# Kernel optimization log

Measured on AMD Instinct MI355X. Metric: run time of the kernel, lower is better.

## Reference

```python
import jax, jax.numpy as jnp
import numpy as np

NR, NQ, NH, NV = 256, 64, 64, 4
B = 8192
NDRAW = 12
# zoneout probabilities from __init__ (applied deterministically, eval-mode expectation)
ZO_IJ, ZO_ID, ZO_GJ, ZO_GD = 0.3, 0.2, 0.3, 0.2


def _lin_init(key, fan_in, fan_out):
    kw, kb = jax.random.split(key)
    s = 1.0 / np.sqrt(fan_in)
    W = jax.random.uniform(kw, (fan_in, fan_out), jnp.float32, -s, s)
    b = jax.random.uniform(kb, (fan_out,), jnp.float32, -s, s)
    return W, b


def setup_inputs() -> dict:
    key = jax.random.key(0)
    ks = jax.random.split(key, 16)
    inp = {"ndraw": NDRAW}
    inp["cnd_repr"] = jax.random.normal(ks[0], (B, NR), jnp.float32)
    inp["qry_jrep"] = jax.random.normal(ks[1], (B, NQ), jnp.float32)
    inp["qry_drep"] = jax.random.normal(ks[2], (B, NQ), jnp.float32)
    inp["qry_v"] = jax.random.normal(ks[3], (B, NV), jnp.float32)
    for n in ["hi_j", "ci_j", "oi_j", "hi_d", "ci_d", "oi_d",
              "hg_j", "cg_j", "og_j", "hg_d", "cg_d", "og_d", "ug_j", "ug_d"]:
        inp[n] = jnp.zeros((B, NH), jnp.float32)
    # LSTM cells: W [in+nh, 4*nh]
    inp["W_ij"], inp["b_ij"] = _lin_init(ks[4], NR + NQ + NH + NH, 4 * NH)
    inp["W_id"], inp["b_id"] = _lin_init(ks[5], NR + NQ + NH + NH, 4 * NH)
    inp["W_gj"], inp["b_gj"] = _lin_init(ks[6], NR + NH + NH, 4 * NH)
    inp["W_gd"], inp["b_gd"] = _lin_init(ks[7], NR + NH + NV + NH, 4 * NH)
    # GaussianFactor heads: nh -> (mean, logv)
    inp["W_poj"], inp["b_poj"] = _lin_init(ks[8], NH, 2 * NH)
    inp["W_pod"], inp["b_pod"] = _lin_init(ks[9], NH, 2 * NH)
    inp["W_prj"], inp["b_prj"] = _lin_init(ks[10], NH, 2 * NH)
    inp["W_prd"], inp["b_prd"] = _lin_init(ks[11], NH, 2 * NH)
    # GeneratorDelta: cat(u, h) -> delta
    inp["W_dj"], inp["b_dj"] = _lin_init(ks[12], 2 * NH, NH)
    inp["W_dd"], inp["b_dd"] = _lin_init(ks[13], 2 * NH, NH)
    return inp


def _lstm(x, h, c, W, b, zo):
    g = jnp.concatenate([x, h], axis=1) @ W + b  # [B, 4*NH]
    i, f, gg, o = jnp.split(g, 4, axis=1)
    i, f, o = jax.nn.sigmoid(i), jax.nn.sigmoid(f), jax.nn.sigmoid(o)
    c_new = f * c + i * jnp.tanh(gg)
    h_new = o * jnp.tanh(c_new)
    # deterministic zoneout (expectation form)
    return zo * h + (1.0 - zo) * h_new, zo * c + (1.0 - zo) * c_new, o


def _gauss_stats(h, W, b):
    s = h @ W + b
    mean, logv = jnp.split(s, 2, axis=1)
    return mean, logv


def _delta(u, h, W, b):
    return jax.nn.leaky_relu(jnp.concatenate([u, h], axis=1) @ W + b)


def _forward(ndraw, cnd_repr, qry_jrep, qry_drep, qry_v,
             hi_j, ci_j, oi_j, hi_d, ci_d, oi_d,
             hg_j, cg_j, og_j, hg_d, cg_d, og_d, ug_j, ug_d,
             W_ij, b_ij, W_id, b_id, W_gj, b_gj, W_gd, b_gd,
             W_poj, b_poj, W_pod, b_pod, W_prj, b_prj, W_prd, b_prd,
             W_dj, b_dj, W_dd, b_dd):
    Bn = cnd_repr.shape[0]
    eps_j = jax.random.normal(jax.random.key(1), (ndraw, Bn, NH), jnp.float32)
    eps_d = jax.random.normal(jax.random.key(2), (ndraw, Bn, NH), jnp.float32)

    def step(carry, eps):
        (hi_j, ci_j, oi_j, hi_d, ci_d, oi_d,
         hg_j, cg_j, og_j, hg_d, cg_d, og_d, ug_j, ug_d) = carry
        ej, ed = eps
        # priors from current generator states (sampled z unused in loop)
        pr_m_j, pr_v_j = _gauss_stats(hg_j, W_prj, b_prj)
        pr_m_d, pr_v_d = _gauss_stats(hg_d, W_prd, b_prd)
        # inference states
        inp_ij = jnp.concatenate([cnd_repr, qry_jrep, hg_j], axis=1)
        inp_id = jnp.concatenate([cnd_repr, qry_drep, hg_d], axis=1)
        hi_j, ci_j, oi_j = _lstm(inp_ij, hi_j, ci_j, W_ij, b_ij, ZO_IJ)
        hi_d, ci_d, oi_d = _lstm(inp_id, hi_d, ci_d, W_id, b_id, ZO_ID)
        # posteriors + reparameterized samples
        po_m_j, po_v_j = _gauss_stats(hi_j, W_poj, b_poj)
        po_m_d, po_v_d = _gauss_stats(hi_d, W_pod, b_pod)
        z_j = po_m_j + jnp.exp(0.5 * po_v_j) * ej
        z_d = po_m_d + jnp.exp(0.5 * po_v_d) * ed
        # generator states
        inp_gj = jnp.concatenate([cnd_repr, z_j], axis=1)
        inp_gd = jnp.concatenate([cnd_repr, z_d, qry_v], axis=1)
        hg_j, cg_j, og_j = _lstm(inp_gj, hg_j, cg_j, W_gj, b_gj, ZO_GJ)
        hg_d, cg_d, og_d = _lstm(inp_gd, hg_d, cg_d, W_gd, b_gd, ZO_GD)
        # additive canvas updates
        ug_j = ug_j + _delta(ug_j, hg_j, W_dj, b_dj)
        ug_d = ug_d + _delta(ug_d, hg_d, W_dd, b_dd)
        carry = (hi_j, ci_j, oi_j, hi_d, ci_d, oi_d,
                 hg_j, cg_j, og_j, hg_d, cg_d, og_d, ug_j, ug_d)
        ys = (pr_m_j, pr_v_j, pr_m_d, pr_v_d, po_m_j, po_v_j, po_m_d, po_v_d)
        return carry, ys

    carry0 = (hi_j, ci_j, oi_j, hi_d, ci_d, oi_d,
              hg_j, cg_j, og_j, hg_d, cg_d, og_d, ug_j, ug_d)
    carry, ys = jax.lax.scan(step, carry0, (eps_j, eps_d))
    ug_j_out, ug_d_out = carry[-2], carry[-1]
    # pack: [2 + 8*ndraw, B, NH] (canvases then per-draw prior/posterior stats)
    out = jnp.concatenate([ug_j_out[None], ug_d_out[None]] + list(ys), axis=0)
    return out


def reference(ndraw, cnd_repr, qry_jrep, qry_drep, qry_v,
              hi_j, ci_j, oi_j, hi_d, ci_d, oi_d,
              hg_j, cg_j, og_j, hg_d, cg_d, og_d, ug_j, ug_d,
              W_ij, b_ij, W_id, b_id, W_gj, b_gj, W_gd, b_gd,
              W_poj, b_poj, W_pod, b_pod, W_prj, b_prj, W_prd, b_prd,
              W_dj, b_dj, W_dd, b_dd):
    return _forward(ndraw, cnd_repr, qry_jrep, qry_drep, qry_v,
                    hi_j, ci_j, oi_j, hi_d, ci_d, oi_d,
                    hg_j, cg_j, og_j, hg_d, cg_d, og_d, ug_j, ug_d,
                    W_ij, b_ij, W_id, b_id, W_gj, b_gj, W_gd, b_gd,
                    W_poj, b_poj, W_pod, b_pod, W_prj, b_prj, W_prd, b_prd,
                    W_dj, b_dj, W_dd, b_dd)
```

## Files before the change

kernel.cpp:

```cpp
#include <hip/hip_runtime.h>
#include <hip/hip_bf16.h>


#define RROWS 16

typedef __attribute__((ext_vector_type(8))) short bf16x8;
typedef __attribute__((ext_vector_type(4))) float f32x4;

#define MFMA(A, Bv, C) __builtin_amdgcn_mfma_f32_16x16x32_bf16(A, Bv, C, 0, 0, 0)

#define FR_WI   0
#define FR_WG   32768
#define FR_WPR  65536
#define FR_WPO  73728
#define FR_WD   81920
#define FR_SIDE 90112

__device__ __forceinline__ unsigned short f2bf(float f) {
  unsigned u = __float_as_uint(f);
  return (unsigned short)((u + 0x7FFFu + ((u >> 16) & 1u)) >> 16);
}
__device__ __forceinline__ unsigned pk2(float a, float b) {
  return (unsigned)f2bf(a) | ((unsigned)f2bf(b) << 16);
}
__device__ __forceinline__ float sigf(float x) {
  return 1.0f / (1.0f + __expf(-x));
}
__device__ __forceinline__ float tanh_f(float x) {
  return 1.0f - 2.0f / (__expf(2.0f * x) + 1.0f);
}

__device__ __forceinline__ float eps_threefry(unsigned seed, unsigned idx) {
  unsigned x0 = 0u, x1 = idx;
  const unsigned ks0 = 0u, ks1 = seed, ks2 = seed ^ 0x1BD11BDAu;
  x0 += ks0; x1 += ks1;
#define TF_R(r) { x0 += x1; x1 = (x1 << (r)) | (x1 >> (32 - (r))); x1 ^= x0; }
  TF_R(13) TF_R(15) TF_R(26) TF_R(6)  x0 += ks1; x1 += ks2 + 1u;
  TF_R(17) TF_R(29) TF_R(16) TF_R(24) x0 += ks2; x1 += ks0 + 2u;
  TF_R(13) TF_R(15) TF_R(26) TF_R(6)  x0 += ks0; x1 += ks1 + 3u;
  TF_R(17) TF_R(29) TF_R(16) TF_R(24) x0 += ks1; x1 += ks2 + 4u;
  TF_R(13) TF_R(15) TF_R(26) TF_R(6)  x0 += ks2; x1 += ks0 + 5u;
#undef TF_R
  unsigned bits = x0 ^ x1;
  unsigned fb = (bits >> 9) | 0x3F800000u;
  const float lo = -0.99999994f;
  float f = __uint_as_float(fb) - 1.0f;
  float u = fmaxf(lo, f * 2.0f + lo);
  float w = -log1pf(-u * u);
  float p;
  if (w < 5.0f) {
    w -= 2.5f;
    p = 2.81022636e-08f;
    p = fmaf(p, w, 3.43273939e-07f);
    p = fmaf(p, w, -3.5233877e-06f);
    p = fmaf(p, w, -4.39150654e-06f);
    p = fmaf(p, w, 0.00021858087f);
    p = fmaf(p, w, -0.00125372503f);
    p = fmaf(p, w, -0.00417768164f);
    p = fmaf(p, w, 0.246640727f);
    p = fmaf(p, w, 1.50140941f);
  } else {
    w = sqrtf(w) - 3.0f;
    p = -0.000200214257f;
    p = fmaf(p, w, 0.000100950558f);
    p = fmaf(p, w, 0.00134934322f);
    p = fmaf(p, w, -0.00367342844f);
    p = fmaf(p, w, 0.00573950773f);
    p = fmaf(p, w, -0.0076224613f);
    p = fmaf(p, w, 0.00943887047f);
    p = fmaf(p, w, 1.00167406f);
    p = fmaf(p, w, 2.83297682f);
  }
  return 1.41421356f * (p * u);
}

__global__ __launch_bounds__(256) void GeRN_eps(float* __restrict__ ebuf,
                                                unsigned ndBN)
{
  unsigned j0 = (blockIdx.x * 256u + threadIdx.x) * 8u;
  const unsigned total = 2u * ndBN;
  if (j0 >= total) return;
  const unsigned s = (j0 >= ndBN) ? 1u : 0u;
  const unsigned i0 = j0 - s * ndBN;
  const unsigned seed = 1u + s;
  float v[8];
  #pragma unroll
  for (int k = 0; k < 8; ++k) v[k] = eps_threefry(seed, i0 + (unsigned)k);
  float4 a = {v[0], v[1], v[2], v[3]};
  float4 b = {v[4], v[5], v[6], v[7]};
  *(float4*)(ebuf + j0) = a;
  *(float4*)(ebuf + j0 + 4) = b;
}

__global__ __launch_bounds__(64) void GeRN_prep(
    const float* __restrict__ Wij, const float* __restrict__ Wid,
    const float* __restrict__ Wgj, const float* __restrict__ Wgd,
    const float* __restrict__ Wprj, const float* __restrict__ Wprd,
    const float* __restrict__ Wpoj, const float* __restrict__ Wpod,
    const float* __restrict__ Wdj, const float* __restrict__ Wdd,
    unsigned short* __restrict__ frB, unsigned short* __restrict__ sBs)
{
  const int l = threadIdx.x;
  if (blockIdx.x < 352) {
    const int s = blockIdx.x / 176;
    int tt = blockIdx.x % 176;
    const float* W; int ldw, rb, NT, kt, nt; size_t doff;
    if (tt < 64)       { W = s ? Wid : Wij; ldw = 256; NT = 16; kt = tt >> 4; nt = tt & 15;
                         rb = 320 + kt * 32; doff = FR_WI; }
    else if (tt < 128) { tt -= 64; W = s ? Wgd : Wgj; ldw = 256; NT = 16; kt = tt >> 4; nt = tt & 15;
                         rb = (kt < 2) ? 256 + kt * 32 : (s ? 324 : 320) + (kt - 2) * 32; doff = FR_WG; }
    else if (tt < 144) { tt -= 128; W = s ? Wprd : Wprj; ldw = 128; NT = 8; kt = tt >> 3; nt = tt & 7;
                         rb = kt * 32; doff = FR_WPR; }
    else if (tt < 160) { tt -= 144; W = s ? Wpod : Wpoj; ldw = 128; NT = 8; kt = tt >> 3; nt = tt & 7;
                         rb = kt * 32; doff = FR_WPO; }
    else               { tt -= 160; W = s ? Wdd : Wdj; ldw = 64; NT = 4; kt = tt >> 2; nt = tt & 3;
                         rb = (kt < 2) ? kt * 32 : 64 + (kt - 2) * 32; doff = FR_WD; }
    unsigned short* dst = frB + (size_t)s * FR_SIDE + doff
                        + ((size_t)(kt * NT + nt) * 64 + l) * 8;
    const int kk = (l >> 4) * 8;
    const int c = nt * 16 + (l & 15);
    #pragma unroll
    for (int j = 0; j < 8; ++j)
      dst[j] = f2bf(W[(size_t)(rb + kk + j) * ldw + c]);
  } else {
    int bb = blockIdx.x - 352;
    int mat, base;
    if (bb < 160)      { mat = 0; base = 0; }
    else if (bb < 320) { mat = 1; base = 160; }
    else if (bb < 448) { mat = 2; base = 320; }
    else               { mat = 3; base = 448; }
    int tt = bb - base;
    int kk = tt >> 4, nt = tt & 15;
    const float* W = mat == 0 ? Wij : mat == 1 ? Wid : mat == 2 ? Wgj : Wgd;
    const int c = nt * 16 + (l & 15);
    const int kl0 = (l >> 4) * 8;
    unsigned short* dst = sBs + ((size_t)bb * 64 + l) * 8;
    if (mat == 3 && kk == 8) {
      #pragma unroll
      for (int j = 0; j < 8; ++j) {
        int klo = kl0 + j;
        dst[j] = (klo < 4) ? f2bf(W[(size_t)(320 + klo) * 256 + c]) : (unsigned short)0;
      }
    } else {
      int rb = (kk < 8) ? kk * 32 : 256 + (kk - 8) * 32;
      #pragma unroll
      for (int j = 0; j < 8; ++j)
        dst[j] = f2bf(W[(size_t)(rb + kl0 + j) * 256 + c]);
    }
  }
}

__global__ __launch_bounds__(256) void GeRN_staticM(
    const float* __restrict__ cnd, const float* __restrict__ qj,
    const float* __restrict__ qd, const float* __restrict__ qv,
    const float* __restrict__ bij, const float* __restrict__ bid,
    const float* __restrict__ bgj, const float* __restrict__ bgd,
    const unsigned short* __restrict__ sBs,
    float* __restrict__ pre, int B)
{
  alignas(16) __shared__ unsigned short As[13][2][64][8];
  const int tid = threadIdx.x;
  const int l = tid & 63;
  const int wv = tid >> 6;
  const int b0 = blockIdx.x * 32;

  for (int i = tid; i < 32 * 52; i += 256) {
    int r = i / 52, kc = i % 52;
    int mf = r >> 4, rr = r & 15;
    float v[8];
    if (kc < 32) {
      const float4* p = (const float4*)&cnd[(size_t)(b0 + r) * 256 + kc * 8];
      float4 x0 = p[0], x1 = p[1];
      v[0] = x0.x; v[1] = x0.y; v[2] = x0.z; v[3] = x0.w;
      v[4] = x1.x; v[5] = x1.y; v[6] = x1.z; v[7] = x1.w;
    } else if (kc < 40) {
      const float4* p = (const float4*)&qj[(size_t)(b0 + r) * 64 + (kc - 32) * 8];
      float4 x0 = p[0], x1 = p[1];
      v[0] = x0.x; v[1] = x0.y; v[2] = x0.z; v[3] = x0.w;
      v[4] = x1.x; v[5] = x1.y; v[6] = x1.z; v[7] = x1.w;
    } else if (kc < 48) {
      const float4* p = (const float4*)&qd[(size_t)(b0 + r) * 64 + (kc - 40) * 8];
      float4 x0 = p[0], x1 = p[1];
      v[0] = x0.x; v[1] = x0.y; v[2] = x0.z; v[3] = x0.w;
      v[4] = x1.x; v[5] = x1.y; v[6] = x1.z; v[7] = x1.w;
    } else if (kc == 48) {
      #pragma unroll
      for (int j = 0; j < 8; ++j) v[j] = (j < 4) ? qv[(size_t)(b0 + r) * 4 + j] : 0.0f;
    } else {
      #pragma unroll
      for (int j = 0; j < 8; ++j) v[j] = 0.0f;
    }
    int kt = kc >> 2;
    int lane = rr + (kc & 3) * 16;
    uint4 wq;
    wq.x = pk2(v[0], v[1]); wq.y = pk2(v[2], v[3]);
    wq.z = pk2(v[4], v[5]); wq.w = pk2(v[6], v[7]);
    *(uint4*)&As[kt][mf][lane][0] = wq;
  }
  __syncthreads();

  const int colb = wv * 64 + (l & 15);
  const int rowb = (l >> 4) * 4;

  #pragma unroll
  for (int mat = 0; mat < 4; ++mat) {
    const int ktN  = (mat == 2) ? 8 : (mat == 3) ? 9 : 10;
    const int ktB  = mat == 0 ? 0 : mat == 1 ? 160 : mat == 2 ? 320 : 448;
    const float* bv = mat == 0 ? bij : mat == 1 ? bid : mat == 2 ? bgj : bgd;
    f32x4 acc[2][4];
    #pragma unroll
    for (int ntl = 0; ntl < 4; ++ntl) {
      float bb = bv[colb + ntl * 16];
      f32x4 s = {bb, bb, bb, bb};
      acc[0][ntl] = s; acc[1][ntl] = s;
    }
    #pragma unroll
    for (int kk = 0; kk < ktN; ++kk) {
      int ktA = (kk < 8) ? kk : (mat == 0 ? kk : mat == 1 ? kk + 2 : 12);
      bf16x8 a0 = *(const bf16x8*)&As[ktA][0][l][0];
      bf16x8 a1 = *(const bf16x8*)&As[ktA][1][l][0];
      #pragma unroll
      for (int ntl = 0; ntl < 4; ++ntl) {
        bf16x8 bf = *(const bf16x8*)&sBs[((size_t)(ktB + kk * 16 + wv * 4 + ntl) * 64 + l) * 8];
        acc[0][ntl] = MFMA(a0, bf, acc[0][ntl]);
        acc[1][ntl] = MFMA(a1, bf, acc[1][ntl]);
      }
    }
    float* dp = pre + (size_t)mat * B * 256;
    #pragma unroll
    for (int mf = 0; mf < 2; ++mf)
      #pragma unroll
      for (int ntl = 0; ntl < 4; ++ntl)
        #pragma unroll
        for (int r = 0; r < 4; ++r)
          dp[(size_t)(b0 + mf * 16 + rowb + r) * 256 + colb + ntl * 16] = acc[mf][ntl][r];
  }
}

#define WR_FR(buf, row, c, v) \
  fr[buf][(c) >> 5][((row) & 15) + (((c) >> 3) & 3) * 16][(c) & 7] = f2bf(v)
#define LD_FR(buf, kt) (*(const bf16x8*)&fr[buf][kt][l][0])
#define LD_B(off, kt, nt, NT) \
  (*(const bf16x8*)(FB + (off) + (((kt) * (NT) + (nt)) * 64 + l) * 8))
#define LD_H(ph, kt, nt) \
  (*(const bf16x8*)&shH[(ph) * 8192 + (((kt) * 8 + (nt)) * 64 + l) * 8])

template<int USE_EPS>
__global__ __launch_bounds__(256, 2) void GeRN_recur(
    const unsigned short* __restrict__ frB,
    const float* __restrict__ pre_ij, const float* __restrict__ pre_id,
    const float* __restrict__ pre_gj, const float* __restrict__ pre_gd,
    const float* __restrict__ bprj, const float* __restrict__ bprd,
    const float* __restrict__ bpoj, const float* __restrict__ bpod,
    const float* __restrict__ bdj,  const float* __restrict__ bdd,
    const float* __restrict__ hi_j0, const float* __restrict__ ci_j0,
    const float* __restrict__ hi_d0, const float* __restrict__ ci_d0,
    const float* __restrict__ hg_j0, const float* __restrict__ cg_j0,
    const float* __restrict__ hg_d0, const float* __restrict__ cg_d0,
    const float* __restrict__ ug_j0, const float* __restrict__ ug_d0,
    const float* __restrict__ eps_buf, unsigned ndBN,
    float* __restrict__ out, int B, int nd)
{
  alignas(16) __shared__ unsigned short fr[6][2][64][8];
  alignas(16) __shared__ float preL[2][4][4][64][4];
  alignas(16) __shared__ unsigned short shH[16384];

  const int tid = threadIdx.x;
  const int l   = tid & 63;
  const int wv  = tid >> 6;
  const int s   = blockIdx.x & 1;
  const int rbk = blockIdx.x >> 1;
  const int r0  = (l >> 4) * 4;
  const int col = wv * 16 + (l & 15);
  const int bbase = rbk * 16;
  const size_t BN = (size_t)B * 64;

  const float* hi0 = s ? hi_d0 : hi_j0;  const float* ci0 = s ? ci_d0 : ci_j0;
  const float* hg0 = s ? hg_d0 : hg_j0;  const float* cg0 = s ? cg_d0 : cg_j0;
  const float* ug0 = s ? ug_d0 : ug_j0;
  const float* preIg = s ? pre_id : pre_ij;
  const float* preGg = s ? pre_gd : pre_gj;
  const float* BPR = s ? bprd : bprj;
  const float* BPO = s ? bpod : bpoj;
  const float* BD  = s ? bdd  : bdj;
  const unsigned short* FB = frB + (size_t)s * FR_SIDE;

  bf16x8 wi[4][4], wg[4][4], wd[4];
  #pragma unroll
  for (int kt = 0; kt < 4; ++kt) {
    #pragma unroll
    for (int g = 0; g < 4; ++g) {
      wi[kt][g] = LD_B(FR_WI, kt, g * 4 + wv, 16);
      wg[kt][g] = LD_B(FR_WG, kt, g * 4 + wv, 16);
    }
    wd[kt] = LD_B(FR_WD, kt, wv, 4);
  }
  {
    const float4* src = (const float4*)(FB + FR_WPR);
    float4* dst = (float4*)shH;
    for (int i = tid; i < 2048; i += 256) dst[i] = src[i];
  }

  float hi_[4], ci_[4], hg_[4], cg_[4], u_[4];
  #pragma unroll
  for (int r = 0; r < 4; ++r) {
    size_t gi = (size_t)(bbase + r0 + r) * 64 + col;
    hi_[r] = hi0[gi]; ci_[r] = ci0[gi];
    hg_[r] = hg0[gi]; cg_[r] = cg0[gi];
    u_[r]  = ug0[gi];
  }
  const float bprm = BPR[col], bprv = BPR[64 + col];
  const float bpom = BPO[col], bpov = BPO[64 + col];
  const float bd   = BD[col];

  #pragma unroll
  for (int g = 0; g < 4; ++g)
    #pragma unroll
    for (int r = 0; r < 4; ++r) {
      preL[0][g][wv][l][r] = preIg[(size_t)(bbase + r0 + r) * 256 + g * 64 + col];
      preL[1][g][wv][l][r] = preGg[(size_t)(bbase + r0 + r) * 256 + g * 64 + col];
    }
  #pragma unroll
  for (int r = 0; r < 4; ++r) {
    WR_FR(0, r0 + r, col, hi_[r]);
    WR_FR(2, r0 + r, col, hg_[r]);
    WR_FR(4, r0 + r, col, u_[r]);
  }
  __syncthreads();

  const float zo = s ? 0.2f : 0.3f, zo1 = 1.0f - zo;

  const unsigned gi0 = (unsigned)((bbase + r0) * 64 + col);
  float* o_prm = out + (size_t)(2 + (2 * s) * nd) * BN + gi0;
  float* o_prv = out + (size_t)(2 + (2 * s + 1) * nd) * BN + gi0;
  float* o_pom = out + (size_t)(2 + (4 + 2 * s) * nd) * BN + gi0;
  float* o_pov = out + (size_t)(2 + (5 + 2 * s) * nd) * BN + gi0;
  unsigned e0 = gi0;
  const unsigned BNu = (unsigned)BN;
  const unsigned eseed = 1u + (unsigned)s;
  const float* ep = USE_EPS ? (eps_buf + (size_t)s * ndBN + gi0) : (const float*)0;

  for (int t = 0; t < nd; ++t) {
    const int cb = t & 1;
    float epre[4];
    if (USE_EPS) {
      #pragma unroll
      for (int r = 0; r < 4; ++r) epre[r] = ep[r * 64];
    }
    bf16x8 a_hg0 = LD_FR(2, 0), a_hg1 = LD_FR(2, 1);
    bf16x8 a_hi0 = LD_FR(cb, 0), a_hi1 = LD_FR(cb, 1);

    {
      f32x4 am = {bprm, bprm, bprm, bprm};
      f32x4 av = {bprv, bprv, bprv, bprv};
      am = MFMA(a_hg0, LD_H(0, 0, wv), am);
      am = MFMA(a_hg1, LD_H(0, 1, wv), am);
      av = MFMA(a_hg0, LD_H(0, 0, wv + 4), av);
      av = MFMA(a_hg1, LD_H(0, 1, wv + 4), av);
      #pragma unroll
      for (int r = 0; r < 4; ++r) {
        o_prm[r * 64] = am[r];
        o_prv[r * 64] = av[r];
      }
    }
    {
      f32x4 acc[4];
      #pragma unroll
      for (int g = 0; g < 4; ++g) acc[g] = *(const f32x4*)&preL[0][g][wv][l][0];
      #pragma unroll
      for (int g = 0; g < 4; ++g) {
        acc[g] = MFMA(a_hg0, wi[0][g], acc[g]);
        acc[g] = MFMA(a_hg1, wi[1][g], acc[g]);
        acc[g] = MFMA(a_hi0, wi[2][g], acc[g]);
        acc[g] = MFMA(a_hi1, wi[3][g], acc[g]);
      }
      #pragma unroll
      for (int r = 0; r < 4; ++r) {
        float ig = sigf(acc[0][r]), fg = sigf(acc[1][r]);
        float gg = tanh_f(acc[2][r]), og = sigf(acc[3][r]);
        float cn = fmaf(fg, ci_[r], ig * gg);
        float hn = og * tanh_f(cn);
        hi_[r] = fmaf(zo, hi_[r], zo1 * hn);
        ci_[r] = fmaf(zo, ci_[r], zo1 * cn);
        WR_FR(cb ^ 1, r0 + r, col, hi_[r]);
      }
    }
    __syncthreads();

    {
      bf16x8 a0 = LD_FR(cb ^ 1, 0), a1 = LD_FR(cb ^ 1, 1);
      f32x4 am = {bpom, bpom, bpom, bpom};
      f32x4 av = {bpov, bpov, bpov, bpov};
      am = MFMA(a0, LD_H(1, 0, wv), am);
      am = MFMA(a1, LD_H(1, 1, wv), am);
      av = MFMA(a0, LD_H(1, 0, wv + 4), av);
      av = MFMA(a1, LD_H(1, 1, wv + 4), av);
      #pragma unroll
      for (int r = 0; r < 4; ++r) {
        o_pom[r * 64] = am[r];
        o_pov[r * 64] = av[r];
        float e = USE_EPS ? epre[r] : eps_threefry(eseed, e0 + r * 64);
        float z = fmaf(__expf(0.5f * av[r]), e, am[r]);
        WR_FR(3, r0 + r, col, z);
      }
    }
    __syncthreads();

    {
      bf16x8 az0 = LD_FR(3, 0), az1 = LD_FR(3, 1);
      f32x4 acc[4];
      #pragma unroll
      for (int g = 0; g < 4; ++g) acc[g] = *(const f32x4*)&preL[1][g][wv][l][0];
      #pragma unroll
      for (int g = 0; g < 4; ++g) {
        acc[g] = MFMA(az0,   wg[0][g], acc[g]);
        acc[g] = MFMA(az1,   wg[1][g], acc[g]);
        acc[g] = MFMA(a_hg0, wg[2][g], acc[g]);
        acc[g] = MFMA(a_hg1, wg[3][g], acc[g]);
      }
      #pragma unroll
      for (int r = 0; r < 4; ++r) {
        float ig = sigf(acc[0][r]), fg = sigf(acc[1][r]);
        float gg = tanh_f(acc[2][r]), og = sigf(acc[3][r]);
        float cn = fmaf(fg, cg_[r], ig * gg);
        float hn = og * tanh_f(cn);
        hg_[r] = fmaf(zo, hg_[r], zo1 * hn);
        cg_[r] = fmaf(zo, cg_[r], zo1 * cn);
        WR_FR(2, r0 + r, col, hg_[r]);
      }
    }
    __syncthreads();

    {
      bf16x8 au0 = LD_FR(4 + cb, 0), au1 = LD_FR(4 + cb, 1);
      bf16x8 ah0 = LD_FR(2, 0), ah1 = LD_FR(2, 1);
      f32x4 acc = {bd, bd, bd, bd};
      acc = MFMA(au0, wd[0], acc);
      acc = MFMA(au1, wd[1], acc);
      acc = MFMA(ah0, wd[2], acc);
      acc = MFMA(ah1, wd[3], acc);
      #pragma unroll
      for (int r = 0; r < 4; ++r) {
        float a = acc[r];
        float d = a > 0.0f ? a : 0.01f * a;
        u_[r] += d;
        WR_FR(4 + (cb ^ 1), r0 + r, col, u_[r]);
      }
    }
    __syncthreads();

    o_prm += BN; o_prv += BN; o_pom += BN; o_pov += BN;
    e0 += BNu;
    if (USE_EPS) ep += BN;
  }

  #pragma unroll
  for (int r = 0; r < 4; ++r) {
    size_t gi = (size_t)(bbase + r0 + r) * 64 + col;
    out[(size_t)s * BN + gi] = u_[r];
  }
}

extern "C" void kernel_launch(void* const* d_in, const int* in_sizes, int n_in,
                              void* d_out, int out_size, void* d_ws, size_t ws_size,
                              hipStream_t stream)
{
  const float* cnd = (const float*)d_in[1];
  const float* qj  = (const float*)d_in[2];
  const float* qd  = (const float*)d_in[3];
  const float* qv  = (const float*)d_in[4];
  const float* hi_j0 = (const float*)d_in[5];
  const float* ci_j0 = (const float*)d_in[6];
  const float* hi_d0 = (const float*)d_in[8];
  const float* ci_d0 = (const float*)d_in[9];
  const float* hg_j0 = (const float*)d_in[11];
  const float* cg_j0 = (const float*)d_in[12];
  const float* hg_d0 = (const float*)d_in[14];
  const float* cg_d0 = (const float*)d_in[15];
  const float* ug_j0 = (const float*)d_in[17];
  const float* ug_d0 = (const float*)d_in[18];
  const float* Wij = (const float*)d_in[19]; const float* bij = (const float*)d_in[20];
  const float* Wid = (const float*)d_in[21]; const float* bid = (const float*)d_in[22];
  const float* Wgj = (const float*)d_in[23]; const float* bgj = (const float*)d_in[24];
  const float* Wgd = (const float*)d_in[25]; const float* bgd = (const float*)d_in[26];
  const float* Wpoj = (const float*)d_in[27]; const float* bpoj = (const float*)d_in[28];
  const float* Wpod = (const float*)d_in[29]; const float* bpod = (const float*)d_in[30];
  const float* Wprj = (const float*)d_in[31]; const float* bprj = (const float*)d_in[32];
  const float* Wprd = (const float*)d_in[33]; const float* bprd = (const float*)d_in[34];
  const float* Wdj = (const float*)d_in[35]; const float* bdj = (const float*)d_in[36];
  const float* Wdd = (const float*)d_in[37]; const float* bdd = (const float*)d_in[38];

  const int B = in_sizes[1] / 256;
  const int slots = out_size / (B * 64);
  const int nd = (slots - 2) / 8;

  float* ws = (float*)d_ws;
  const size_t preBytes = (size_t)4 * B * 256 * 4;
  unsigned short* frB = (unsigned short*)((char*)d_ws + preBytes);
  unsigned short* sBs = frB + 2 * FR_SIDE;
  size_t epsOff = preBytes + (size_t)2 * FR_SIDE * 2 + (size_t)592 * 512 * 2;
  epsOff = (epsOff + 255) & ~(size_t)255;
  const unsigned ndBN = (unsigned)((size_t)nd * B * 64);
  float* epsBuf = (float*)((char*)d_ws + epsOff);
  const bool useEps = ws_size >= epsOff + (size_t)2 * ndBN * 4;
  float* out = (float*)d_out;

  GeRN_prep<<<944, 64, 0, stream>>>(
      Wij, Wid, Wgj, Wgd, Wprj, Wprd, Wpoj, Wpod, Wdj, Wdd, frB, sBs);
  if (useEps) {
    GeRN_eps<<<(int)((2u * ndBN + 2047u) / 2048u), 256, 0, stream>>>(epsBuf, ndBN);
  }
  GeRN_staticM<<<B / 32, 256, 0, stream>>>(
      cnd, qj, qd, qv, bij, bid, bgj, bgd, sBs, ws, B);
  if (useEps) {
    GeRN_recur<1><<<2 * (B / 16), 256, 0, stream>>>(
        frB,
        ws, ws + (size_t)B * 256, ws + (size_t)2 * B * 256, ws + (size_t)3 * B * 256,
        bprj, bprd, bpoj, bpod, bdj, bdd,
        hi_j0, ci_j0, hi_d0, ci_d0, hg_j0, cg_j0, hg_d0, cg_d0, ug_j0, ug_d0,
        epsBuf, ndBN, out, B, nd);
  } else {
    GeRN_recur<0><<<2 * (B / 16), 256, 0, stream>>>(
        frB,
        ws, ws + (size_t)B * 256, ws + (size_t)2 * B * 256, ws + (size_t)3 * B * 256,
        bprj, bprd, bpoj, bpod, bdj, bdd,
        hi_j0, ci_j0, hi_d0, ci_d0, hg_j0, cg_j0, hg_d0, cg_d0, ug_j0, ug_d0,
        (const float*)0, ndBN, out, B, nd);
  }
}
```

Measured before the change: 232.0 us.

## Merge prep and eps kernels; double rows per recurrent block with 512 threads

The weight-prep and epsilon-generation kernels become one launch with 256-thread blocks, removing a launch. The recurrent kernel now handles 32 rows per block using 8 waves split into two row halves. Each half gets its own shared fragment and preactivation buffers, while the projection and delta weights are shared through LDS. The delta weights move from registers to LDS to lower register pressure. In exchange, block-wide barriers now synchronize twice as many waves, shared memory per block grows, and occupancy may change.

```diff
diff --git a/kernel.cpp b/kernel.cpp
--- a/kernel.cpp
+++ b/kernel.cpp
@@ -74,79 +74,79 @@
   return 1.41421356f * (p * u);
 }
 
-__global__ __launch_bounds__(256) void GeRN_eps(float* __restrict__ ebuf,
-                                                unsigned ndBN)
-{
-  unsigned j0 = (blockIdx.x * 256u + threadIdx.x) * 8u;
-  const unsigned total = 2u * ndBN;
-  if (j0 >= total) return;
-  const unsigned s = (j0 >= ndBN) ? 1u : 0u;
-  const unsigned i0 = j0 - s * ndBN;
-  const unsigned seed = 1u + s;
-  float v[8];
-  #pragma unroll
-  for (int k = 0; k < 8; ++k) v[k] = eps_threefry(seed, i0 + (unsigned)k);
-  float4 a = {v[0], v[1], v[2], v[3]};
-  float4 b = {v[4], v[5], v[6], v[7]};
-  *(float4*)(ebuf + j0) = a;
-  *(float4*)(ebuf + j0 + 4) = b;
-}
-
-__global__ __launch_bounds__(64) void GeRN_prep(
+__global__ __launch_bounds__(256) void GeRN_prepEps(
     const float* __restrict__ Wij, const float* __restrict__ Wid,
     const float* __restrict__ Wgj, const float* __restrict__ Wgd,
     const float* __restrict__ Wprj, const float* __restrict__ Wprd,
     const float* __restrict__ Wpoj, const float* __restrict__ Wpod,
     const float* __restrict__ Wdj, const float* __restrict__ Wdd,
-    unsigned short* __restrict__ frB, unsigned short* __restrict__ sBs)
+    unsigned short* __restrict__ frB, unsigned short* __restrict__ sBs,
+    float* __restrict__ ebuf, unsigned ndBN)
 {
-  const int l = threadIdx.x;
-  if (blockIdx.x < 352) {
-    const int s = blockIdx.x / 176;
-    int tt = blockIdx.x % 176;
-    const float* W; int ldw, rb, NT, kt, nt; size_t doff;
-    if (tt < 64)       { W = s ? Wid : Wij; ldw = 256; NT = 16; kt = tt >> 4; nt = tt & 15;
-                         rb = 320 + kt * 32; doff = FR_WI; }
-    else if (tt < 128) { tt -= 64; W = s ? Wgd : Wgj; ldw = 256; NT = 16; kt = tt >> 4; nt = tt & 15;
-                         rb = (kt < 2) ? 256 + kt * 32 : (s ? 324 : 320) + (kt - 2) * 32; doff = FR_WG; }
-    else if (tt < 144) { tt -= 128; W = s ? Wprd : Wprj; ldw = 128; NT = 8; kt = tt >> 3; nt = tt & 7;
-                         rb = kt * 32; doff = FR_WPR; }
-    else if (tt < 160) { tt -= 144; W = s ? Wpod : Wpoj; ldw = 128; NT = 8; kt = tt >> 3; nt = tt & 7;
-                         rb = kt * 32; doff = FR_WPO; }
-    else               { tt -= 160; W = s ? Wdd : Wdj; ldw = 64; NT = 4; kt = tt >> 2; nt = tt & 3;
-                         rb = (kt < 2) ? kt * 32 : 64 + (kt - 2) * 32; doff = FR_WD; }
-    unsigned short* dst = frB + (size_t)s * FR_SIDE + doff
-                        + ((size_t)(kt * NT + nt) * 64 + l) * 8;
-    const int kk = (l >> 4) * 8;
-    const int c = nt * 16 + (l & 15);
+  if (blockIdx.x < 236) {
+    const int vb = blockIdx.x * 4 + (threadIdx.x >> 6);
+    const int l = threadIdx.x & 63;
+    if (vb < 352) {
+      const int s = vb / 176;
+      int tt = vb % 176;
+      const float* W; int ldw, rb, NT, kt, nt; size_t doff;
+      if (tt < 64)       { W = s ? Wid : Wij; ldw = 256; NT = 16; kt = tt >> 4; nt = tt & 15;
+                           rb = 320 + kt * 32; doff = FR_WI; }
+      else if (tt < 128) { tt -= 64; W = s ? Wgd : Wgj; ldw = 256; NT = 16; kt = tt >> 4; nt = tt & 15;
+                           rb = (kt < 2) ? 256 + kt * 32 : (s ? 324 : 320) + (kt - 2) * 32; doff = FR_WG; }
+      else if (tt < 144) { tt -= 128; W = s ? Wprd : Wprj; ldw = 128; NT = 8; kt = tt >> 3; nt = tt & 7;
+                           rb = kt * 32; doff = FR_WPR; }
+      else if (tt < 160) { tt -= 144; W = s ? Wpod : Wpoj; ldw = 128; NT = 8; kt = tt >> 3; nt = tt & 7;
+                           rb = kt * 32; doff = FR_WPO; }
+      else               { tt -= 160; W = s ? Wdd : Wdj; ldw = 64; NT = 4; kt = tt >> 2; nt = tt & 3;
+                           rb = (kt < 2) ? kt * 32 : 64 + (kt - 2) * 32; doff = FR_WD; }
+      unsigned short* dst = frB + (size_t)s * FR_SIDE + doff
+                          + ((size_t)(kt * NT + nt) * 64 + l) * 8;
+      const int kk = (l >> 4) * 8;
+      const int c = nt * 16 + (l & 15);
+      #pragma unroll
+      for (int j = 0; j < 8; ++j)
+        dst[j] = f2bf(W[(size_t)(rb + kk + j) * ldw + c]);
+    } else {
+      int bb = vb - 352;
+      int mat, base;
+      if (bb < 160)      { mat = 0; base = 0; }
+      else if (bb < 320) { mat = 1; base = 160; }
+      else if (bb < 448) { mat = 2; base = 320; }
+      else               { mat = 3; base = 448; }
+      int tt = bb - base;
+      int kk = tt >> 4, nt = tt & 15;
+      const float* W = mat == 0 ? Wij : mat == 1 ? Wid : mat == 2 ? Wgj : Wgd;
+      const int c = nt * 16 + (l & 15);
+      const int kl0 = (l >> 4) * 8;
+      unsigned short* dst = sBs + ((size_t)bb * 64 + l) * 8;
+      if (mat == 3 && kk == 8) {
+        #pragma unroll
+        for (int j = 0; j < 8; ++j) {
+          int klo = kl0 + j;
+          dst[j] = (klo < 4) ? f2bf(W[(size_t)(320 + klo) * 256 + c]) : (unsigned short)0;
+        }
+      } else {
+        int rb = (kk < 8) ? kk * 32 : 256 + (kk - 8) * 32;
+        #pragma unroll
+        for (int j = 0; j < 8; ++j)
+          dst[j] = f2bf(W[(size_t)(rb + kl0 + j) * 256 + c]);
+      }
+    }
+  } else {
+    unsigned j0 = ((blockIdx.x - 236) * 256u + threadIdx.x) * 8u;
+    const unsigned total = 2u * ndBN;
+    if (j0 >= total) return;
+    const unsigned s = (j0 >= ndBN) ? 1u : 0u;
+    const unsigned i0 = j0 - s * ndBN;
+    const unsigned seed = 1u + s;
+    float v[8];
     #pragma unroll
-    for (int j = 0; j < 8; ++j)
-      dst[j] = f2bf(W[(size_t)(rb + kk + j) * ldw + c]);
-  } else {
-    int bb = blockIdx.x - 352;
-    int mat, base;
-    if (bb < 160)      { mat = 0; base = 0; }
-    else if (bb < 320) { mat = 1; base = 160; }
-    else if (bb < 448) { mat = 2; base = 320; }
-    else               { mat = 3; base = 448; }
-    int tt = bb - base;
-    int kk = tt >> 4, nt = tt & 15;
-    const float* W = mat == 0 ? Wij : mat == 1 ? Wid : mat == 2 ? Wgj : Wgd;
-    const int c = nt * 16 + (l & 15);
-    const int kl0 = (l >> 4) * 8;
-    unsigned short* dst = sBs + ((size_t)bb * 64 + l) * 8;
-    if (mat == 3 && kk == 8) {
-      #pragma unroll
-      for (int j = 0; j < 8; ++j) {
-        int klo = kl0 + j;
-        dst[j] = (klo < 4) ? f2bf(W[(size_t)(320 + klo) * 256 + c]) : (unsigned short)0;
-      }
-    } else {
-      int rb = (kk < 8) ? kk * 32 : 256 + (kk - 8) * 32;
-      #pragma unroll
-      for (int j = 0; j < 8; ++j)
-        dst[j] = f2bf(W[(size_t)(rb + kl0 + j) * 256 + c]);
-    }
+    for (int k = 0; k < 8; ++k) v[k] = eps_threefry(seed, i0 + (unsigned)k);
+    float4 a = {v[0], v[1], v[2], v[3]};
+    float4 b = {v[4], v[5], v[6], v[7]};
+    *(float4*)(ebuf + j0) = a;
+    *(float4*)(ebuf + j0 + 4) = b;
   }
 }
 
@@ -238,15 +238,15 @@
 }
 
 #define WR_FR(buf, row, c, v) \
-  fr[buf][(c) >> 5][((row) & 15) + (((c) >> 3) & 3) * 16][(c) & 7] = f2bf(v)
-#define LD_FR(buf, kt) (*(const bf16x8*)&fr[buf][kt][l][0])
+  fr[rh][buf][(c) >> 5][((row) & 15) + (((c) >> 3) & 3) * 16][(c) & 7] = f2bf(v)
+#define LD_FR(buf, kt) (*(const bf16x8*)&fr[rh][buf][kt][l][0])
 #define LD_B(off, kt, nt, NT) \
   (*(const bf16x8*)(FB + (off) + (((kt) * (NT) + (nt)) * 64 + l) * 8))
 #define LD_H(ph, kt, nt) \
   (*(const bf16x8*)&shH[(ph) * 8192 + (((kt) * 8 + (nt)) * 64 + l) * 8])
 
 template<int USE_EPS>
-__global__ __launch_bounds__(256, 2) void GeRN_recur(
+__global__ __launch_bounds__(512, 2) void GeRN_recur(
     const unsigned short* __restrict__ frB,
     const float* __restrict__ pre_ij, const float* __restrict__ pre_id,
     const float* __restrict__ pre_gj, const float* __restrict__ pre_gd,
@@ -261,18 +261,21 @@
     const float* __restrict__ eps_buf, unsigned ndBN,
     float* __restrict__ out, int B, int nd)
 {
-  alignas(16) __shared__ unsigned short fr[6][2][64][8];
-  alignas(16) __shared__ float preL[2][4][4][64][4];
+  alignas(16) __shared__ unsigned short fr[2][6][2][64][8];
+  alignas(16) __shared__ float preL[2][2][4][4][64][4];
   alignas(16) __shared__ unsigned short shH[16384];
+  alignas(16) __shared__ unsigned short wdL[4][4][64][8];
 
   const int tid = threadIdx.x;
   const int l   = tid & 63;
-  const int wv  = tid >> 6;
+  const int w   = tid >> 6;
+  const int rh  = w >> 2;
+  const int ws  = w & 3;
   const int s   = blockIdx.x & 1;
   const int rbk = blockIdx.x >> 1;
   const int r0  = (l >> 4) * 4;
-  const int col = wv * 16 + (l & 15);
-  const int bbase = rbk * 16;
+  const int col = ws * 16 + (l & 15);
+  const int bbase = rbk * 32 + rh * 16;
   const size_t BN = (size_t)B * 64;
 
   const float* hi0 = s ? hi_d0 : hi_j0;  const float* ci0 = s ? ci_d0 : ci_j0;
@@ -285,20 +288,21 @@
   const float* BD  = s ? bdd  : bdj;
   const unsigned short* FB = frB + (size_t)s * FR_SIDE;
 
-  bf16x8 wi[4][4], wg[4][4], wd[4];
+  bf16x8 wi[4][4], wg[4][4];
   #pragma unroll
-  for (int kt = 0; kt < 4; ++kt) {
+  for (int kt = 0; kt < 4; ++kt)
     #pragma unroll
     for (int g = 0; g < 4; ++g) {
-      wi[kt][g] = LD_B(FR_WI, kt, g * 4 + wv, 16);
-      wg[kt][g] = LD_B(FR_WG, kt, g * 4 + wv, 16);
-    }
-    wd[kt] = LD_B(FR_WD, kt, wv, 4);
-  }
+      wi[kt][g] = LD_B(FR_WI, kt, g * 4 + ws, 16);
+      wg[kt][g] = LD_B(FR_WG, kt, g * 4 + ws, 16);
+    }
   {
-    const float4* src = (const float4*)(FB + FR_WPR);
-    float4* dst = (float4*)shH;
-    for (int i = tid; i < 2048; i += 256) dst[i] = src[i];
+    const uint4* srcH = (const uint4*)(FB + FR_WPR);
+    uint4* dstH = (uint4*)shH;
+    for (int i = tid; i < 2048; i += 512) dstH[i] = srcH[i];
+    const uint4* srcD = (const uint4*)(FB + FR_WD);
+    uint4* dstD = (uint4*)wdL;
+    for (int i = tid; i < 1024; i += 512) dstD[i] = srcD[i];
   }
 
   float hi_[4], ci_[4], hg_[4], cg_[4], u_[4];
@@ -317,8 +321,8 @@
   for (int g = 0; g < 4; ++g)
     #pragma unroll
     for (int r = 0; r < 4; ++r) {
-      preL[0][g][wv][l][r] = preIg[(size_t)(bbase + r0 + r) * 256 + g * 64 + col];
-      preL[1][g][wv][l][r] = preGg[(size_t)(bbase + r0 + r) * 256 + g * 64 + col];
+      preL[rh][0][g][ws][l][r] = preIg[(size_t)(bbase + r0 + r) * 256 + g * 64 + col];
+      preL[rh][1][g][ws][l][r] = preGg[(size_t)(bbase + r0 + r) * 256 + g * 64 + col];
     }
   #pragma unroll
   for (int r = 0; r < 4; ++r) {
@@ -353,10 +357,10 @@
     {
       f32x4 am = {bprm, bprm, bprm, bprm};
       f32x4 av = {bprv, bprv, bprv, bprv};
-      am = MFMA(a_hg0, LD_H(0, 0, wv), am);
-      am = MFMA(a_hg1, LD_H(0, 1, wv), am);
-      av = MFMA(a_hg0, LD_H(0, 0, wv + 4), av);
-      av = MFMA(a_hg1, LD_H(0, 1, wv + 4), av);
+      am = MFMA(a_hg0, LD_H(0, 0, ws), am);
+      am = MFMA(a_hg1, LD_H(0, 1, ws), am);
+      av = MFMA(a_hg0, LD_H(0, 0, ws + 4), av);
+      av = MFMA(a_hg1, LD_H(0, 1, ws + 4), av);
       #pragma unroll
       for (int r = 0; r < 4; ++r) {
         o_prm[r * 64] = am[r];
@@ -366,7 +370,7 @@
     {
       f32x4 acc[4];
       #pragma unroll
-      for (int g = 0; g < 4; ++g) acc[g] = *(const f32x4*)&preL[0][g][wv][l][0];
+      for (int g = 0; g < 4; ++g) acc[g] = *(const f32x4*)&preL[rh][0][g][ws][l][0];
       #pragma unroll
       for (int g = 0; g < 4; ++g) {
         acc[g] = MFMA(a_hg0, wi[0][g], acc[g]);
@@ -391,10 +395,10 @@
       bf16x8 a0 = LD_FR(cb ^ 1, 0), a1 = LD_FR(cb ^ 1, 1);
       f32x4 am = {bpom, bpom, bpom, bpom};
       f32x4 av = {bpov, bpov, bpov, bpov};
-      am = MFMA(a0, LD_H(1, 0, wv), am);
-      am = MFMA(a1, LD_H(1, 1, wv), am);
-      av = MFMA(a0, LD_H(1, 0, wv + 4), av);
-      av = MFMA(a1, LD_H(1, 1, wv + 4), av);
+      am = MFMA(a0, LD_H(1, 0, ws), am);
+      am = MFMA(a1, LD_H(1, 1, ws), am);
+      av = MFMA(a0, LD_H(1, 0, ws + 4), av);
+      av = MFMA(a1, LD_H(1, 1, ws + 4), av);
       #pragma unroll
       for (int r = 0; r < 4; ++r) {
         o_pom[r * 64] = am[r];
@@ -410,7 +414,7 @@
       bf16x8 az0 = LD_FR(3, 0), az1 = LD_FR(3, 1);
       f32x4 acc[4];
       #pragma unroll
-      for (int g = 0; g < 4; ++g) acc[g] = *(const f32x4*)&preL[1][g][wv][l][0];
+      for (int g = 0; g < 4; ++g) acc[g] = *(const f32x4*)&preL[rh][1][g][ws][l][0];
       #pragma unroll
       for (int g = 0; g < 4; ++g) {
         acc[g] = MFMA(az0,   wg[0][g], acc[g]);
@@ -435,10 +439,10 @@
       bf16x8 au0 = LD_FR(4 + cb, 0), au1 = LD_FR(4 + cb, 1);
       bf16x8 ah0 = LD_FR(2, 0), ah1 = LD_FR(2, 1);
       f32x4 acc = {bd, bd, bd, bd};
-      acc = MFMA(au0, wd[0], acc);
-      acc = MFMA(au1, wd[1], acc);
-      acc = MFMA(ah0, wd[2], acc);
-      acc = MFMA(ah1, wd[3], acc);
+      acc = MFMA(au0, *(const bf16x8*)&wdL[0][ws][l][0], acc);
+      acc = MFMA(au1, *(const bf16x8*)&wdL[1][ws][l][0], acc);
+      acc = MFMA(ah0, *(const bf16x8*)&wdL[2][ws][l][0], acc);
+      acc = MFMA(ah1, *(const bf16x8*)&wdL[3][ws][l][0], acc);
       #pragma unroll
       for (int r = 0; r < 4; ++r) {
         float a = acc[r];
@@ -505,22 +509,21 @@
   const bool useEps = ws_size >= epsOff + (size_t)2 * ndBN * 4;
   float* out = (float*)d_out;
 
-  GeRN_prep<<<944, 64, 0, stream>>>(
-      Wij, Wid, Wgj, Wgd, Wprj, Wprd, Wpoj, Wpod, Wdj, Wdd, frB, sBs);
-  if (useEps) {
-    GeRN_eps<<<(int)((2u * ndBN + 2047u) / 2048u), 256, 0, stream>>>(epsBuf, ndBN);
-  }
+  const int epsBlocks = useEps ? (int)((2u * ndBN + 2047u) / 2048u) : 0;
+  GeRN_prepEps<<<236 + epsBlocks, 256, 0, stream>>>(
+      Wij, Wid, Wgj, Wgd, Wprj, Wprd, Wpoj, Wpod, Wdj, Wdd, frB, sBs,
+      epsBuf, ndBN);
   GeRN_staticM<<<B / 32, 256, 0, stream>>>(
       cnd, qj, qd, qv, bij, bid, bgj, bgd, sBs, ws, B);
   if (useEps) {
-    GeRN_recur<1><<<2 * (B / 16), 256, 0, stream>>>(
+    GeRN_recur<1><<<2 * (B / 32), 512, 0, stream>>>(
         frB,
         ws, ws + (size_t)B * 256, ws + (size_t)2 * B * 256, ws + (size_t)3 * B * 256,
         bprj, bprd, bpoj, bpod, bdj, bdd,
         hi_j0, ci_j0, hi_d0, ci_d0, hg_j0, cg_j0, hg_d0, cg_d0, ug_j0, ug_d0,
         epsBuf, ndBN, out, B, nd);
   } else {
-    GeRN_recur<0><<<2 * (B / 16), 256, 0, stream>>>(
+    GeRN_recur<0><<<2 * (B / 32), 512, 0, stream>>>(
         frB,
         ws, ws + (size_t)B * 256, ws + (size_t)2 * B * 256, ws + (size_t)3 * B * 256,
         bprj, bprd, bpoj, bpod, bdj, bdd,
```

Result: slower. 237.7 us (+2.5%).
